# Optimization experiments

Hardware: AMD Instinct MI355X
Metric: run time of the kernel (lower is better)

## Reference

```python
import jax, jax.numpy as jnp
import numpy as np


def _rnn_scan(x_pre, W_hh, b_hh, h0):
    # x_pre: [S, B, H] precomputed input projection; returns stacked h: [S, B, H]
    def step(h, xp):
        h = jnp.tanh(xp + h @ W_hh.T + b_hh)
        return h, h
    _, hs = jax.lax.scan(step, h0, x_pre)
    return hs


def setup_inputs() -> dict:
    key = jax.random.key(0)
    ks = jax.random.split(key, 12)
    B, S, E, H, V = 16, 256, 512, 1024, 32000
    sE, sH = 1.0 / np.sqrt(E), 1.0 / np.sqrt(H)
    return {
        "x_ids": jax.random.randint(ks[0], (B, S), 0, V),
        "emb": jax.random.normal(ks[1], (V, E), jnp.float32),
        "W_ih1": jax.random.normal(ks[2], (H, E), jnp.float32) * sE,
        "b_ih1": jax.random.normal(ks[3], (H,), jnp.float32) * sH,
        "W_hh1": jax.random.normal(ks[4], (H, H), jnp.float32) * sH,
        "b_hh1": jax.random.normal(ks[5], (H,), jnp.float32) * sH,
        "W_ih2": jax.random.normal(ks[6], (H, H), jnp.float32) * sH,
        "b_ih2": jax.random.normal(ks[7], (H,), jnp.float32) * sH,
        "W_hh2": jax.random.normal(ks[8], (H, H), jnp.float32) * sH,
        "b_hh2": jax.random.normal(ks[9], (H,), jnp.float32) * sH,
        "W_fc": jax.random.normal(ks[10], (V, H), jnp.float32) * sH,
        "b_fc": jax.random.normal(ks[11], (V,), jnp.float32) * sH,
    }


def reference(x_ids, emb, W_ih1, b_ih1, W_hh1, b_hh1, W_ih2, b_ih2, W_hh2, b_hh2, W_fc, b_fc):
    B, S = x_ids.shape
    H = W_hh1.shape[0]
    x = emb[x_ids]  # [B, S, E]
    # layer 1: precompute input projection for all steps, scan over time
    x1 = jnp.einsum('bse,he->sbh', x, W_ih1) + b_ih1  # [S, B, H]
    h0 = jnp.zeros((B, H), x.dtype)
    h1s = _rnn_scan(x1, W_hh1, b_hh1, h0)  # [S, B, H]
    # layer 2
    x2 = jnp.einsum('sbh,gh->sbg', h1s, W_ih2) + b_ih2
    h2s = _rnn_scan(x2, W_hh2, b_hh2, h0)  # [S, B, H]
    # per-step fc + softmax, vectorized
    logits = jnp.einsum('sbh,vh->bsv', h2s, W_fc) + b_fc  # [B, S, V]
    return jax.nn.softmax(logits, axis=-1)
```

## Files before the change

### kernel.cpp

```cpp
#include <hip/hip_runtime.h>
#include <cstdint>
#include <cstddef>

typedef unsigned short u16;
typedef __attribute__((ext_vector_type(4))) float f32x4;
typedef __attribute__((ext_vector_type(8))) short s16x8;
typedef __attribute__((ext_vector_type(8))) unsigned short u16x8;
typedef __attribute__((ext_vector_type(4))) unsigned short u16x4;

#define B_ 16
#define S_ 256
#define E_ 512
#define H_ 1024
#define V_ 32000
#define M_TOK (S_*B_)

__device__ __forceinline__ u16 f2bf(float f) {
  union { float f; unsigned u; } x; x.f = f;
  unsigned r = x.u + 0x7fffu + ((x.u >> 16) & 1u);
  return (u16)(r >> 16);
}

__device__ __forceinline__ void sc_load16(s16x8& d, const u16* p) {
  asm volatile("global_load_dwordx4 %0, %1, off sc0 sc1" : "=v"(d) : "v"(p));
}
__device__ __forceinline__ void sc_load16f(f32x4& d, const float* p) {
  asm volatile("global_load_dwordx4 %0, %1, off sc0 sc1" : "=v"(d) : "v"(p));
}
__device__ __forceinline__ void sc_store8(u16* p, u16x4 v) {
  asm volatile("global_store_dwordx2 %0, %1, off sc0 sc1" :: "v"(p), "v"(v) : "memory");
}
__device__ __forceinline__ void sc_store16f(float* p, f32x4 v) {
  asm volatile("global_store_dwordx4 %0, %1, off sc0 sc1" :: "v"(p), "v"(v) : "memory");
}
__device__ __forceinline__ void wait_vm0() {
  asm volatile("s_waitcnt vmcnt(0)" ::: "memory");
}

__global__ __launch_bounds__(256) void k_cvt(const float* __restrict__ src,
                                             u16* __restrict__ dst, int n4) {
  int i = blockIdx.x*blockDim.x + threadIdx.x;
  int stride = gridDim.x*blockDim.x;
  for (; i < n4; i += stride) {
    float4 v = reinterpret_cast<const float4*>(src)[i];
    ushort4 o;
    o.x = f2bf(v.x); o.y = f2bf(v.y); o.z = f2bf(v.z); o.w = f2bf(v.w);
    reinterpret_cast<ushort4*>(dst)[i] = o;
  }
}

__global__ __launch_bounds__(256) void k_embed(const int* __restrict__ ids,
                                               const float* __restrict__ emb,
                                               u16* __restrict__ A1) {
  int g = blockIdx.x*256 + threadIdx.x;
  int m = g >> 6;
  int c = g & 63;
  int s = m >> 4, b = m & 15;
  int id = ids[b*S_ + s];
  const float4* src = reinterpret_cast<const float4*>(emb + (size_t)id*E_ + (size_t)c*8);
  float4 v0 = src[0], v1 = src[1];
  u16x8 o;
  o[0]=f2bf(v0.x); o[1]=f2bf(v0.y); o[2]=f2bf(v0.z); o[3]=f2bf(v0.w);
  o[4]=f2bf(v1.x); o[5]=f2bf(v1.y); o[6]=f2bf(v1.z); o[7]=f2bf(v1.w);
  *reinterpret_cast<u16x8*>(A1 + (size_t)m*E_ + (size_t)c*8) = o;
}

#define BM 128
#define BN 128
#define BK 32

__device__ __forceinline__ void gload_lds16(const u16* g, u16* l) {
  __builtin_amdgcn_global_load_lds(
      (const __attribute__((address_space(1))) void*)g,
      (__attribute__((address_space(3))) void*)l,
      16, 0, 0);
}

template<int FCMODE>
__global__ __launch_bounds__(256)
void k_gemm(const u16* __restrict__ A, const u16* __restrict__ Bw,
            float* __restrict__ C, const float* __restrict__ bias,
            int M, int N, int K)
{
  __shared__ u16 lA[2][BM*BK];
  __shared__ u16 lB[2][BN*BK];
  const int tid = threadIdx.x;
  const int l = tid & 63, w = tid >> 6;

  const int nwg = gridDim.x * gridDim.y;
  int flat = blockIdx.y * gridDim.x + blockIdx.x;
  flat = (flat & 7) * (nwg >> 3) + (flat >> 3);
  const int m0 = (flat / gridDim.x) * BM;
  const int n0 = (flat % gridDim.x) * BN;

  const int wr = w >> 1, wc = w & 1;

  const int L0 = (w*2+0)*64 + l;
  const int L1 = (w*2+1)*64 + l;
  const int r0 = L0 >> 2, r1 = L1 >> 2;
  const int c0 = (L0 & 3) ^ ((r0 >> 1) & 3);
  const int c1 = (L1 & 3) ^ ((r1 >> 1) & 3);
  const u16* gA0 = A  + (size_t)(m0 + r0)*K + c0*8;
  const u16* gA1 = A  + (size_t)(m0 + r1)*K + c1*8;
  const u16* gB0 = Bw + (size_t)(n0 + r0)*K + c0*8;
  const u16* gB1 = Bw + (size_t)(n0 + r1)*K + c1*8;

  const int fr = l & 15;
  const int xc = (l >> 4) ^ ((fr >> 1) & 3);
  int aoff[4], boff[4];
#pragma unroll
  for (int f = 0; f < 4; ++f) {
    aoff[f] = (wr*64 + f*16 + fr) * BK + xc*8;
    boff[f] = (wc*64 + f*16 + fr) * BK + xc*8;
  }

  f32x4 acc[4][4] = {};
  const int KT = K / BK;

  gload_lds16(gA0, &lA[0][(w*2+0)*512]);
  gload_lds16(gA1, &lA[0][(w*2+1)*512]);
  gload_lds16(gB0, &lB[0][(w*2+0)*512]);
  gload_lds16(gB1, &lB[0][(w*2+1)*512]);
  __syncthreads();

  for (int kt = 0; kt < KT; ++kt) {
    const int buf = kt & 1;
    if (kt + 1 < KT) {
      const int koff = (kt+1)*BK;
      gload_lds16(gA0 + koff, &lA[buf^1][(w*2+0)*512]);
      gload_lds16(gA1 + koff, &lA[buf^1][(w*2+1)*512]);
      gload_lds16(gB0 + koff, &lB[buf^1][(w*2+0)*512]);
      gload_lds16(gB1 + koff, &lB[buf^1][(w*2+1)*512]);
    }
    s16x8 af[4], bq[4];
#pragma unroll
    for (int f = 0; f < 4; ++f) af[f] = *reinterpret_cast<const s16x8*>(&lA[buf][aoff[f]]);
#pragma unroll
    for (int f = 0; f < 4; ++f) bq[f] = *reinterpret_cast<const s16x8*>(&lB[buf][boff[f]]);
#pragma unroll
    for (int fm = 0; fm < 4; ++fm)
#pragma unroll
      for (int fn = 0; fn < 4; ++fn)
        acc[fm][fn] = __builtin_amdgcn_mfma_f32_16x16x32_bf16(af[fm], bq[fn], acc[fm][fn], 0, 0, 0);
    __syncthreads();
  }

  const int rowb = (l >> 4) * 4;
  const int colb = l & 15;
#pragma unroll
  for (int fm = 0; fm < 4; ++fm) {
#pragma unroll
    for (int fn = 0; fn < 4; ++fn) {
      const int col = n0 + wc*64 + fn*16 + colb;
#pragma unroll
      for (int r = 0; r < 4; ++r) {
        const int row = m0 + wr*64 + fm*16 + rowb + r;
        float v = acc[fm][fn][r];
        if (FCMODE) {
          const int b = row & 15, s = row >> 4;
          C[((size_t)(b*S_ + s))*N + col] = v + bias[col];
        } else {
          C[(size_t)row*N + col] = v;
        }
      }
    }
  }
}

__global__ __launch_bounds__(256, 1)
void k_scan3(const u16* __restrict__ Whh1, const u16* __restrict__ Wih2,
             const u16* __restrict__ Whh2, const float* __restrict__ x1,
             const float* __restrict__ bih1, const float* __restrict__ bhh1,
             const float* __restrict__ bih2, const float* __restrict__ bhh2,
             u16* __restrict__ h1s, u16* __restrict__ h2s,
             float* __restrict__ u2s)
{
  __shared__ u16 sh[B_*H_];
  const int tid = threadIdx.x;
  const int l = tid & 63, w = tid >> 6;
  const int role = blockIdx.x >> 4;
  const int blk  = blockIdx.x & 15;
  const int rowA = blk*64 + w*16 + (l & 15);
  const int kc = l >> 4;
  const int bcol = l & 15;
  const int i0 = blk*64 + w*16 + kc*4;

  const u16* Wsel = (role == 0) ? Whh1 : (role == 1) ? Wih2 : Whh2;
  s16x8 wf[32];
  {
    const u16* wp = Wsel + (size_t)rowA*H_ + kc*8;
#pragma unroll
    for (int ks = 0; ks < 32; ++ks) wf[ks] = *reinterpret_cast<const s16x8*>(wp + ks*32);
  }

  auto stage = [&](const u16* src) {
    s16x8 stg[8];
#pragma unroll
    for (int r = 0; r < 8; ++r) sc_load16(stg[r], src + (size_t)(tid + r*256)*8);
    wait_vm0();
    for (;;) {
      unsigned dirty = 0;
#pragma unroll
      for (int r = 0; r < 8; ++r) {
        bool bad = false;
#pragma unroll
        for (int j = 0; j < 8; ++j) bad |= (((unsigned)(unsigned short)stg[r][j]) == 0xFFFFu);
        if (bad) dirty |= (1u << r);
      }
      if (!dirty) break;
#pragma unroll
      for (int r = 0; r < 8; ++r)
        if (dirty & (1u << r)) sc_load16(stg[r], src + (size_t)(tid + r*256)*8);
      wait_vm0();
    }
#pragma unroll
    for (int r = 0; r < 8; ++r) {
      int idx8 = tid + r*256;
      int bt = idx8 >> 7, c8 = idx8 & 127;
      *reinterpret_cast<s16x8*>(reinterpret_cast<char*>(sh) +
          bt*2048 + ((c8*16) ^ ((bt & 7) << 4))) = stg[r];
    }
  };

  const int swz = (bcol & 7) << 4;
  auto hfrag = [&](int ks) -> s16x8 {
    return *reinterpret_cast<const s16x8*>(
        reinterpret_cast<const char*>(sh) + bcol*2048 + (((kc*16) + ks*64) ^ swz));
  };
  auto mfma32 = [&](f32x4& a0, f32x4& a1, f32x4& a2, f32x4& a3) {
#pragma unroll
    for (int ks = 0; ks < 32; ks += 4) {
      a0 = __builtin_amdgcn_mfma_f32_16x16x32_bf16(wf[ks+0], hfrag(ks+0), a0, 0, 0, 0);
      a1 = __builtin_amdgcn_mfma_f32_16x16x32_bf16(wf[ks+1], hfrag(ks+1), a1, 0, 0, 0);
      a2 = __builtin_amdgcn_mfma_f32_16x16x32_bf16(wf[ks+2], hfrag(ks+2), a2, 0, 0, 0);
      a3 = __builtin_amdgcn_mfma_f32_16x16x32_bf16(wf[ks+3], hfrag(ks+3), a3, 0, 0, 0);
    }
  };

  if (role == 0) {
    float bc[4];
#pragma unroll
    for (int r = 0; r < 4; ++r) bc[r] = bih1[i0+r] + bhh1[i0+r];
    float4 xv = *reinterpret_cast<const float4*>(x1 + (size_t)bcol*H_ + i0);
    for (int t = 0; t < S_; ++t) {
      f32x4 a0 = {}, a1 = {}, a2 = {}, a3 = {};
      if (t > 0) {
        stage(h1s + (size_t)(t-1)*(B_*H_));
        __syncthreads();
        mfma32(a0, a1, a2, a3);
      }
      float4 xvn = xv;
      if (t + 1 < S_)
        xvn = *reinterpret_cast<const float4*>(x1 + (size_t)((t+1)*B_ + bcol)*H_ + i0);
      f32x4 tot = (a0 + a1) + (a2 + a3);
      u16x4 o;
      o[0] = f2bf(tanhf(tot[0] + xv.x + bc[0]));
      o[1] = f2bf(tanhf(tot[1] + xv.y + bc[1]));
      o[2] = f2bf(tanhf(tot[2] + xv.z + bc[2]));
      o[3] = f2bf(tanhf(tot[3] + xv.w + bc[3]));
      sc_store8(h1s + (size_t)(t*B_ + bcol)*H_ + i0, o);
      __syncthreads();
      xv = xvn;
    }
  } else if (role == 1) {
    float bc[4];
#pragma unroll
    for (int r = 0; r < 4; ++r) bc[r] = bih2[i0+r] + bhh2[i0+r];
    for (int t = 0; t < S_; ++t) {
      stage(h1s + (size_t)t*(B_*H_));
      __syncthreads();
      f32x4 a0 = {}, a1 = {}, a2 = {}, a3 = {};
      mfma32(a0, a1, a2, a3);
      f32x4 tot = (a0 + a1) + (a2 + a3);
      tot[0] += bc[0]; tot[1] += bc[1]; tot[2] += bc[2]; tot[3] += bc[3];
      sc_store16f(u2s + ((size_t)t*B_ + bcol)*H_ + i0, tot);
      __syncthreads();
    }
  } else {
    for (int t = 0; t < S_; ++t) {
      f32x4 a0 = {}, a1 = {}, a2 = {}, a3 = {};
      if (t > 0) stage(h2s + (size_t)(t-1)*(B_*H_));
      const float* up = u2s + ((size_t)t*B_ + bcol)*H_ + i0;
      f32x4 uv;
      sc_load16f(uv, up);
      wait_vm0();
      for (;;) {
        bool bad = false;
#pragma unroll
        for (int j = 0; j < 4; ++j) bad |= (__float_as_uint(uv[j]) == 0xFFFFFFFFu);
        if (!bad) break;
        sc_load16f(uv, up);
        wait_vm0();
      }
      if (t > 0) {
        __syncthreads();
        mfma32(a0, a1, a2, a3);
      }
      f32x4 tot = (a0 + a1) + (a2 + a3);
      u16x4 o;
      o[0] = f2bf(tanhf(tot[0] + uv[0]));
      o[1] = f2bf(tanhf(tot[1] + uv[1]));
      o[2] = f2bf(tanhf(tot[2] + uv[2]));
      o[3] = f2bf(tanhf(tot[3] + uv[3]));
      sc_store8(h2s + (size_t)(t*B_ + bcol)*H_ + i0, o);
      __syncthreads();
    }
  }
}

__global__ __launch_bounds__(256)
void k_softmax(float* __restrict__ out) {
  const int gw = (blockIdx.x*256 + threadIdx.x) >> 6;
  const int l = threadIdx.x & 63;
  float* row = out + (size_t)gw*V_;
  float m = -3.4e38f, s = 0.f;
  for (int it = 0; it < 125; ++it) {
    float4 v = reinterpret_cast<const float4*>(row)[it*64 + l];
    float cm = fmaxf(fmaxf(v.x, v.y), fmaxf(v.z, v.w));
    float nm = fmaxf(m, cm);
    s = s*__expf(m - nm) + __expf(v.x-nm) + __expf(v.y-nm) + __expf(v.z-nm) + __expf(v.w-nm);
    m = nm;
  }
#pragma unroll
  for (int o = 32; o; o >>= 1) {
    float m2 = __shfl_xor(m, o), s2 = __shfl_xor(s, o);
    float nm = fmaxf(m, m2);
    s = s*__expf(m - nm) + s2*__expf(m2 - nm);
    m = nm;
  }
  const float inv = 1.f / s;
  for (int it = 0; it < 125; ++it) {
    float4 v = reinterpret_cast<const float4*>(row)[it*64 + l];
    float4 p;
    p.x = __expf(v.x - m)*inv; p.y = __expf(v.y - m)*inv;
    p.z = __expf(v.z - m)*inv; p.w = __expf(v.w - m)*inv;
    reinterpret_cast<float4*>(row)[it*64 + l] = p;
  }
}

extern "C" void kernel_launch(void* const* d_in, const int* in_sizes, int n_in,
                              void* d_out, int out_size, void* d_ws, size_t ws_size,
                              hipStream_t stream) {
  (void)in_sizes; (void)n_in; (void)out_size; (void)ws_size;
  const int*   x_ids = (const int*)  d_in[0];
  const float* emb   = (const float*)d_in[1];
  const float* Wih1  = (const float*)d_in[2];
  const float* bih1  = (const float*)d_in[3];
  const float* Whh1  = (const float*)d_in[4];
  const float* bhh1  = (const float*)d_in[5];
  const float* Wih2  = (const float*)d_in[6];
  const float* bih2  = (const float*)d_in[7];
  const float* Whh2  = (const float*)d_in[8];
  const float* bhh2  = (const float*)d_in[9];
  const float* Wfc   = (const float*)d_in[10];
  const float* bfc   = (const float*)d_in[11];
  float* out = (float*)d_out;

  char* ws = (char*)d_ws;
  size_t off = 0;
  auto alloc = [&](size_t bytes) {
    char* p = ws + off; off += (bytes + 255) & ~(size_t)255; return p;
  };
  char* regionA = alloc((size_t)M_TOK*H_*4);
  float* u2s  = (float*)regionA;
  u16* A1     = (u16*)regionA;
  u16* Wih1b  = (u16*)(regionA + (size_t)M_TOK*E_*2);
  u16* Whh1b  = (u16*) alloc((size_t)H_*H_*2);
  u16* Wih2b  = (u16*) alloc((size_t)H_*H_*2);
  u16* Whh2b  = (u16*) alloc((size_t)H_*H_*2);
  u16* Wfcb   = (u16*) alloc((size_t)V_*H_*2);
  float* x1   = (float*)alloc((size_t)M_TOK*H_*4);
  u16* h1s    = (u16*) alloc((size_t)M_TOK*H_*2);
  u16* h2s    = (u16*) alloc((size_t)M_TOK*H_*2);

  k_cvt<<<256,  256, 0, stream>>>(Wih1, Wih1b, H_*E_/4);
  k_cvt<<<256,  256, 0, stream>>>(Whh1, Whh1b, H_*H_/4);
  k_cvt<<<256,  256, 0, stream>>>(Wih2, Wih2b, H_*H_/4);
  k_cvt<<<256,  256, 0, stream>>>(Whh2, Whh2b, H_*H_/4);
  k_cvt<<<2048, 256, 0, stream>>>(Wfc,  Wfcb,  V_*H_/4);
  k_embed<<<M_TOK*64/256, 256, 0, stream>>>(x_ids, emb, A1);

  k_gemm<0><<<dim3(H_/BN, M_TOK/BM), 256, 0, stream>>>(A1, Wih1b, x1, nullptr, M_TOK, H_, E_);

  hipMemsetAsync(u2s, 0xFF, (size_t)M_TOK*H_*4, stream);
  hipMemsetAsync(h1s, 0xFF, (size_t)M_TOK*H_*2, stream);
  hipMemsetAsync(h2s, 0xFF, (size_t)M_TOK*H_*2, stream);
  k_scan3<<<48, 256, 0, stream>>>(Whh1b, Wih2b, Whh2b, x1,
                                  bih1, bhh1, bih2, bhh2, h1s, h2s, u2s);

  k_gemm<1><<<dim3(V_/BN, M_TOK/BM), 256, 0, stream>>>(h2s, Wfcb, out, bfc, M_TOK, V_, H_);
  k_softmax<<<M_TOK/4, 256, 0, stream>>>(out);
}
```

Baseline: 1.886 ms.

## Replace sentinel-value polling with per-block flag arrays and store intermediates in bf16

The recurrent scan now synchronises producer and consumer blocks through small per-timestep flag arrays instead of memsetting whole h1s/u2s/h2s buffers to 0xFF and re-polling the data for sentinel values. This removes three large memsets and the retry loops over staged data. Intermediate x1 and u2 buffers become bf16, which halves their traffic but adds rounding error. The GEMM tile order is also remapped to N-major. The added wait_vm0 before each flag store puts store latency on the critical path of every step.

```diff
diff --git a/kernel.cpp b/kernel.cpp
--- a/kernel.cpp
+++ b/kernel.cpp
@@ -14,24 +14,35 @@
 #define H_ 1024
 #define V_ 32000
 #define M_TOK (S_*B_)
+#define BH (B_*H_)
 
 __device__ __forceinline__ u16 f2bf(float f) {
   union { float f; unsigned u; } x; x.f = f;
   unsigned r = x.u + 0x7fffu + ((x.u >> 16) & 1u);
   return (u16)(r >> 16);
 }
+__device__ __forceinline__ float bf2f(u16 x) {
+  union { unsigned u; float f; } c; c.u = ((unsigned)x) << 16; return c.f;
+}
 
 __device__ __forceinline__ void sc_load16(s16x8& d, const u16* p) {
   asm volatile("global_load_dwordx4 %0, %1, off sc0 sc1" : "=v"(d) : "v"(p));
 }
-__device__ __forceinline__ void sc_load16f(f32x4& d, const float* p) {
-  asm volatile("global_load_dwordx4 %0, %1, off sc0 sc1" : "=v"(d) : "v"(p));
+__device__ __forceinline__ void sc_load8w(u16x4& d, const u16* p) {
+  asm volatile("global_load_dwordx2 %0, %1, off sc0 sc1\n\ts_waitcnt vmcnt(0)"
+               : "=v"(d) : "v"(p) : "memory");
+}
+__device__ __forceinline__ int sc_load4w(const int* p) {
+  int d;
+  asm volatile("global_load_dword %0, %1, off sc0 sc1\n\ts_waitcnt vmcnt(0)"
+               : "=v"(d) : "v"(p) : "memory");
+  return d;
 }
 __device__ __forceinline__ void sc_store8(u16* p, u16x4 v) {
   asm volatile("global_store_dwordx2 %0, %1, off sc0 sc1" :: "v"(p), "v"(v) : "memory");
 }
-__device__ __forceinline__ void sc_store16f(float* p, f32x4 v) {
-  asm volatile("global_store_dwordx4 %0, %1, off sc0 sc1" :: "v"(p), "v"(v) : "memory");
+__device__ __forceinline__ void sc_store4(int* p, int v) {
+  asm volatile("global_store_dword %0, %1, off sc0 sc1" :: "v"(p), "v"(v) : "memory");
 }
 __device__ __forceinline__ void wait_vm0() {
   asm volatile("s_waitcnt vmcnt(0)" ::: "memory");
@@ -88,10 +99,10 @@
   const int l = tid & 63, w = tid >> 6;
 
   const int nwg = gridDim.x * gridDim.y;
-  int flat = blockIdx.y * gridDim.x + blockIdx.x;
-  flat = (flat & 7) * (nwg >> 3) + (flat >> 3);
-  const int m0 = (flat / gridDim.x) * BM;
-  const int n0 = (flat % gridDim.x) * BN;
+  int d = blockIdx.y * gridDim.x + blockIdx.x;
+  int tt = (d & 7) * (nwg >> 3) + (d >> 3);
+  const int n0 = (tt / gridDim.y) * BN;
+  const int m0 = (tt % gridDim.y) * BM;
 
   const int wr = w >> 1, wc = w & 1;
 
@@ -156,9 +167,11 @@
       for (int r = 0; r < 4; ++r) {
         const int row = m0 + wr*64 + fm*16 + rowb + r;
         float v = acc[fm][fn][r];
-        if (FCMODE) {
+        if (FCMODE == 1) {
           const int b = row & 15, s = row >> 4;
           C[((size_t)(b*S_ + s))*N + col] = v + bias[col];
+        } else if (FCMODE == 2) {
+          ((u16*)C)[(size_t)row*N + col] = f2bf(v);
         } else {
           C[(size_t)row*N + col] = v;
         }
@@ -168,14 +181,14 @@
 }
 
 __global__ __launch_bounds__(256, 1)
-void k_scan3(const u16* __restrict__ Whh1, const u16* __restrict__ Wih2,
-             const u16* __restrict__ Whh2, const float* __restrict__ x1,
+void k_scan5(const u16* __restrict__ Whh1, const u16* __restrict__ Wih2,
+             const u16* __restrict__ Whh2, const u16* __restrict__ x1b,
              const float* __restrict__ bih1, const float* __restrict__ bhh1,
              const float* __restrict__ bih2, const float* __restrict__ bhh2,
-             u16* __restrict__ h1s, u16* __restrict__ h2s,
-             float* __restrict__ u2s)
+             u16* __restrict__ h1s, u16* __restrict__ u2s, u16* __restrict__ h2s,
+             int* __restrict__ s1, int* __restrict__ su, int* __restrict__ s2)
 {
-  __shared__ u16 sh[B_*H_];
+  __shared__ u16 sh[BH];
   const int tid = threadIdx.x;
   const int l = tid & 63, w = tid >> 6;
   const int role = blockIdx.x >> 4;
@@ -184,6 +197,7 @@
   const int kc = l >> 4;
   const int bcol = l & 15;
   const int i0 = blk*64 + w*16 + kc*4;
+  const int jme = (tid & 127) >> 3;
 
   const u16* Wsel = (role == 0) ? Whh1 : (role == 1) ? Wih2 : Whh2;
   s16x8 wf[32];
@@ -193,26 +207,12 @@
     for (int ks = 0; ks < 32; ++ks) wf[ks] = *reinterpret_cast<const s16x8*>(wp + ks*32);
   }
 
-  auto stage = [&](const u16* src) {
+  auto stage = [&](const u16* src, const int* sentrow) {
+    while (sc_load4w(sentrow + jme) != 0) __builtin_amdgcn_s_sleep(2);
     s16x8 stg[8];
 #pragma unroll
     for (int r = 0; r < 8; ++r) sc_load16(stg[r], src + (size_t)(tid + r*256)*8);
     wait_vm0();
-    for (;;) {
-      unsigned dirty = 0;
-#pragma unroll
-      for (int r = 0; r < 8; ++r) {
-        bool bad = false;
-#pragma unroll
-        for (int j = 0; j < 8; ++j) bad |= (((unsigned)(unsigned short)stg[r][j]) == 0xFFFFu);
-        if (bad) dirty |= (1u << r);
-      }
-      if (!dirty) break;
-#pragma unroll
-      for (int r = 0; r < 8; ++r)
-        if (dirty & (1u << r)) sc_load16(stg[r], src + (size_t)(tid + r*256)*8);
-      wait_vm0();
-    }
 #pragma unroll
     for (int r = 0; r < 8; ++r) {
       int idx8 = tid + r*256;
@@ -241,69 +241,66 @@
     float bc[4];
 #pragma unroll
     for (int r = 0; r < 4; ++r) bc[r] = bih1[i0+r] + bhh1[i0+r];
-    float4 xv = *reinterpret_cast<const float4*>(x1 + (size_t)bcol*H_ + i0);
     for (int t = 0; t < S_; ++t) {
       f32x4 a0 = {}, a1 = {}, a2 = {}, a3 = {};
       if (t > 0) {
-        stage(h1s + (size_t)(t-1)*(B_*H_));
+        stage(h1s + (size_t)(t-1)*BH, s1 + (t-1)*16);
         __syncthreads();
         mfma32(a0, a1, a2, a3);
       }
-      float4 xvn = xv;
-      if (t + 1 < S_)
-        xvn = *reinterpret_cast<const float4*>(x1 + (size_t)((t+1)*B_ + bcol)*H_ + i0);
+      u16x4 xr = *reinterpret_cast<const u16x4*>(x1b + (size_t)(t*B_ + bcol)*H_ + i0);
       f32x4 tot = (a0 + a1) + (a2 + a3);
       u16x4 o;
-      o[0] = f2bf(tanhf(tot[0] + xv.x + bc[0]));
-      o[1] = f2bf(tanhf(tot[1] + xv.y + bc[1]));
-      o[2] = f2bf(tanhf(tot[2] + xv.z + bc[2]));
-      o[3] = f2bf(tanhf(tot[3] + xv.w + bc[3]));
+      o[0] = f2bf(tanhf(tot[0] + bf2f(xr[0]) + bc[0]));
+      o[1] = f2bf(tanhf(tot[1] + bf2f(xr[1]) + bc[1]));
+      o[2] = f2bf(tanhf(tot[2] + bf2f(xr[2]) + bc[2]));
+      o[3] = f2bf(tanhf(tot[3] + bf2f(xr[3]) + bc[3]));
       sc_store8(h1s + (size_t)(t*B_ + bcol)*H_ + i0, o);
-      __syncthreads();
-      xv = xvn;
+      wait_vm0();
+      __syncthreads();
+      if (tid == 0) sc_store4(s1 + t*16 + blk, 0);
     }
   } else if (role == 1) {
     float bc[4];
 #pragma unroll
     for (int r = 0; r < 4; ++r) bc[r] = bih2[i0+r] + bhh2[i0+r];
     for (int t = 0; t < S_; ++t) {
-      stage(h1s + (size_t)t*(B_*H_));
+      stage(h1s + (size_t)t*BH, s1 + t*16);
       __syncthreads();
       f32x4 a0 = {}, a1 = {}, a2 = {}, a3 = {};
       mfma32(a0, a1, a2, a3);
       f32x4 tot = (a0 + a1) + (a2 + a3);
-      tot[0] += bc[0]; tot[1] += bc[1]; tot[2] += bc[2]; tot[3] += bc[3];
-      sc_store16f(u2s + ((size_t)t*B_ + bcol)*H_ + i0, tot);
-      __syncthreads();
+      u16x4 o;
+      o[0] = f2bf(tot[0] + bc[0]);
+      o[1] = f2bf(tot[1] + bc[1]);
+      o[2] = f2bf(tot[2] + bc[2]);
+      o[3] = f2bf(tot[3] + bc[3]);
+      sc_store8(u2s + (size_t)(t*B_ + bcol)*H_ + i0, o);
+      wait_vm0();
+      __syncthreads();
+      if (tid == 0) sc_store4(su + t*16 + blk, 0);
     }
   } else {
     for (int t = 0; t < S_; ++t) {
+      if (tid == 0) {
+        while (sc_load4w(su + t*16 + blk) != 0) __builtin_amdgcn_s_sleep(2);
+      }
+      if (t > 0) stage(h2s + (size_t)(t-1)*BH, s2 + (t-1)*16);
+      __syncthreads();
+      u16x4 uv;
+      sc_load8w(uv, u2s + (size_t)(t*B_ + bcol)*H_ + i0);
       f32x4 a0 = {}, a1 = {}, a2 = {}, a3 = {};
-      if (t > 0) stage(h2s + (size_t)(t-1)*(B_*H_));
-      const float* up = u2s + ((size_t)t*B_ + bcol)*H_ + i0;
-      f32x4 uv;
-      sc_load16f(uv, up);
-      wait_vm0();
-      for (;;) {
-        bool bad = false;
-#pragma unroll
-        for (int j = 0; j < 4; ++j) bad |= (__float_as_uint(uv[j]) == 0xFFFFFFFFu);
-        if (!bad) break;
-        sc_load16f(uv, up);
-        wait_vm0();
-      }
-      if (t > 0) {
-        __syncthreads();
-        mfma32(a0, a1, a2, a3);
-      }
+      if (t > 0) mfma32(a0, a1, a2, a3);
       f32x4 tot = (a0 + a1) + (a2 + a3);
       u16x4 o;
-      o[0] = f2bf(tanhf(tot[0] + uv[0]));
-      o[1] = f2bf(tanhf(tot[1] + uv[1]));
-      o[2] = f2bf(tanhf(tot[2] + uv[2]));
-      o[3] = f2bf(tanhf(tot[3] + uv[3]));
+      o[0] = f2bf(tanhf(tot[0] + bf2f(uv[0])));
+      o[1] = f2bf(tanhf(tot[1] + bf2f(uv[1])));
+      o[2] = f2bf(tanhf(tot[2] + bf2f(uv[2])));
+      o[3] = f2bf(tanhf(tot[3] + bf2f(uv[3])));
       sc_store8(h2s + (size_t)(t*B_ + bcol)*H_ + i0, o);
-      __syncthreads();
+      wait_vm0();
+      __syncthreads();
+      if (tid == 0) sc_store4(s2 + t*16 + blk, 0);
     }
   }
 }
@@ -361,17 +358,18 @@
   auto alloc = [&](size_t bytes) {
     char* p = ws + off; off += (bytes + 255) & ~(size_t)255; return p;
   };
-  char* regionA = alloc((size_t)M_TOK*H_*4);
-  float* u2s  = (float*)regionA;
-  u16* A1     = (u16*)regionA;
-  u16* Wih1b  = (u16*)(regionA + (size_t)M_TOK*E_*2);
+  int* sent   = (int*) alloc(3 * S_ * 16 * 4);
+  u16* Wfcb   = (u16*) alloc((size_t)V_*H_*2);
   u16* Whh1b  = (u16*) alloc((size_t)H_*H_*2);
   u16* Wih2b  = (u16*) alloc((size_t)H_*H_*2);
   u16* Whh2b  = (u16*) alloc((size_t)H_*H_*2);
-  u16* Wfcb   = (u16*) alloc((size_t)V_*H_*2);
-  float* x1   = (float*)alloc((size_t)M_TOK*H_*4);
+  u16* x1b    = (u16*) alloc((size_t)M_TOK*H_*2);
   u16* h1s    = (u16*) alloc((size_t)M_TOK*H_*2);
+  u16* u2s    = (u16*) alloc((size_t)M_TOK*H_*2);
   u16* h2s    = (u16*) alloc((size_t)M_TOK*H_*2);
+  u16* A1     = (u16*) alloc((size_t)M_TOK*E_*2);
+  u16* Wih1b  = (u16*) alloc((size_t)H_*E_*2);
+  int* s1 = sent, *su = sent + S_*16, *s2 = sent + 2*S_*16;
 
   k_cvt<<<256,  256, 0, stream>>>(Wih1, Wih1b, H_*E_/4);
   k_cvt<<<256,  256, 0, stream>>>(Whh1, Whh1b, H_*H_/4);
@@ -380,13 +378,12 @@
   k_cvt<<<2048, 256, 0, stream>>>(Wfc,  Wfcb,  V_*H_/4);
   k_embed<<<M_TOK*64/256, 256, 0, stream>>>(x_ids, emb, A1);
 
-  k_gemm<0><<<dim3(H_/BN, M_TOK/BM), 256, 0, stream>>>(A1, Wih1b, x1, nullptr, M_TOK, H_, E_);
-
-  hipMemsetAsync(u2s, 0xFF, (size_t)M_TOK*H_*4, stream);
-  hipMemsetAsync(h1s, 0xFF, (size_t)M_TOK*H_*2, stream);
-  hipMemsetAsync(h2s, 0xFF, (size_t)M_TOK*H_*2, stream);
-  k_scan3<<<48, 256, 0, stream>>>(Whh1b, Wih2b, Whh2b, x1,
-                                  bih1, bhh1, bih2, bhh2, h1s, h2s, u2s);
+  k_gemm<2><<<dim3(H_/BN, M_TOK/BM), 256, 0, stream>>>(A1, Wih1b, (float*)x1b, nullptr, M_TOK, H_, E_);
+
+  hipMemsetAsync(sent, 0xFF, 3 * S_ * 16 * 4, stream);
+  k_scan5<<<48, 256, 0, stream>>>(Whh1b, Wih2b, Whh2b, x1b,
+                                  bih1, bhh1, bih2, bhh2,
+                                  h1s, u2s, h2s, s1, su, s2);
 
   k_gemm<1><<<dim3(V_/BN, M_TOK/BM), 256, 0, stream>>>(h2s, Wfcb, out, bfc, M_TOK, V_, H_);
   k_softmax<<<M_TOK/4, 256, 0, stream>>>(out);
```

New measurement: 1.935 ms. 1.03x slower.
